# Performance work log

Measured on AMD Instinct MI355X. Metric: run time of the kernel, lower is better.

Reference implementation:

```python
import jax, jax.numpy as jnp
import numpy as np

N = 50000      # atoms
E = 800000     # edges (avg degree 32)
H = 64         # hidden_channels
F = 64         # num_filters
G = 50         # num_gaussians
L = 6          # num_interactions
B = 128        # graphs in batch
MAX_Z = 100
CUTOFF = 10.0


def setup_inputs() -> dict:
    key = jax.random.key(0)
    ks = jax.random.split(key, 20)
    s = 0.05  # weight scale
    return {
        "z": jax.random.randint(ks[0], (N,), 0, MAX_Z, dtype=jnp.int32),
        "pos": jax.random.uniform(ks[1], (N, 3), dtype=jnp.float32) * 5.0,
        "batch": jnp.sort(jax.random.randint(ks[2], (N,), 0, B, dtype=jnp.int32)),
        "edge_index": jax.random.randint(ks[3], (2, E), 0, N, dtype=jnp.int32),
        "embed": jax.random.normal(ks[4], (MAX_Z, H), dtype=jnp.float32) * s,
        "mlp_w1": jax.random.normal(ks[5], (L, G, F), dtype=jnp.float32) * s,
        "mlp_b1": jax.random.normal(ks[6], (L, F), dtype=jnp.float32) * s,
        "mlp_w2": jax.random.normal(ks[7], (L, F, F), dtype=jnp.float32) * s,
        "mlp_b2": jax.random.normal(ks[8], (L, F), dtype=jnp.float32) * s,
        "lin_w": jax.random.normal(ks[9], (L, H, F), dtype=jnp.float32) * s,
        "lin_out_w": jax.random.normal(ks[10], (L, F, H), dtype=jnp.float32) * s,
        "lin_out_b": jax.random.normal(ks[11], (L, H), dtype=jnp.float32) * s,
        "fc1_w": jax.random.normal(ks[12], (H, H // 2), dtype=jnp.float32) * s,
        "fc1_b": jax.random.normal(ks[13], (H // 2,), dtype=jnp.float32) * s,
        "fc2_w": jax.random.normal(ks[14], (H // 2, 1), dtype=jnp.float32) * s,
        "fc2_b": jax.random.normal(ks[15], (1,), dtype=jnp.float32) * s,
    }


def reference(z, pos, batch, edge_index, embed, mlp_w1, mlp_b1, mlp_w2, mlp_b2,
              lin_w, lin_out_w, lin_out_b, fc1_w, fc1_b, fc2_w, fc2_b):
    src, dst = edge_index[0], edge_index[1]
    # edge distances (replaces the python cdist loop; edge list is precomputed)
    d = jnp.sqrt(jnp.sum((pos[src] - pos[dst]) ** 2, axis=-1))  # [E]
    # Gaussian smearing
    offset = jnp.linspace(0.0, CUTOFF, G)
    coeff = -0.5 / (offset[1] - offset[0]) ** 2
    edge_attr = jnp.exp(coeff * (d[:, None] - offset) ** 2)  # [E, G]
    # cosine cutoff
    cut = 0.5 * (jnp.cos(d * np.pi / CUTOFF) + 1.0) * (d < CUTOFF).astype(d.dtype)  # [E]

    h = embed[z]  # [N, H]
    for l in range(L):
        # filter MLP on edge features, modulated by cutoff
        W = jnp.tanh(edge_attr @ mlp_w1[l] + mlp_b1[l]) @ mlp_w2[l] + mlp_b2[l]  # [E, F]
        W = W * cut[:, None]
        h_j = h @ lin_w[l]  # [N, F]
        messages = h_j[src] * W  # gather + modulate  [E, F]
        agg = jax.ops.segment_sum(messages, dst, num_segments=N)  # scatter-add [N, F]
        h = h + (agg @ lin_out_w[l] + lin_out_b[l])  # residual

    # global mean pool over graphs
    sums = jax.ops.segment_sum(h, batch, num_segments=B)  # [B, H]
    cnt = jax.ops.segment_sum(jnp.ones((h.shape[0],), h.dtype), batch, num_segments=B)
    pooled = sums / jnp.maximum(cnt, 1.0)[:, None]

    x = jax.nn.relu(pooled @ fc1_w + fc1_b)  # dropout = identity (eval)
    return x @ fc2_w + fc2_b  # [B, 1]
```

## Files before the change

kernel.cpp:

```cpp
#include <hip/hip_runtime.h>
#include <hip/hip_fp16.h>
#include <math.h>

#define E_EDGES 800000
#define N_ATOMS 50000
#define N_GRAPH 128
#define P_TBL   2048
#define SCAN_NB 49

static constexpr float PI_F   = 3.14159265358979323846f;
static constexpr float GSTEP  = 10.0f / 49.0f;
static constexpr float GCOEFF = -0.5f / (GSTEP * GSTEP);
static constexpr float DMAX   = 8.6603f;
static constexpr float DSCALE = (float)(P_TBL - 1) / DMAX;

__global__ void hist_kernel(const int* __restrict__ dst, int* __restrict__ cnt) {
    int e = blockIdx.x * 256 + threadIdx.x;
    if (e < E_EDGES) atomicAdd(&cnt[dst[e]], 1);
}

__global__ __launch_bounds__(1024)
void scan1_kernel(const int* __restrict__ cnt, int* __restrict__ local_ex,
                  int* __restrict__ bsum) {
    __shared__ int sh[1024];
    const int t = threadIdx.x;
    const int i = blockIdx.x * 1024 + t;
    const int v = (i < N_ATOMS) ? cnt[i] : 0;
    sh[t] = v;
    __syncthreads();
    #pragma unroll
    for (int off = 1; off < 1024; off <<= 1) {
        int u = (t >= off) ? sh[t - off] : 0;
        __syncthreads();
        sh[t] += u;
        __syncthreads();
    }
    if (i < N_ATOMS) local_ex[i] = sh[t] - v;
    if (t == 1023) bsum[blockIdx.x] = sh[t];
}

__global__ __launch_bounds__(1024)
void scan2_kernel(const int* __restrict__ local_ex, const int* __restrict__ bsum,
                  int* __restrict__ starts, int* __restrict__ cursor) {
    __shared__ int off;
    const int b = blockIdx.x;
    if (threadIdx.x < 64) {
        int v = (threadIdx.x < b) ? bsum[threadIdx.x] : 0;
        #pragma unroll
        for (int d = 32; d > 0; d >>= 1) v += __shfl_down(v, d, 64);
        if (threadIdx.x == 0) off = v;
    }
    __syncthreads();
    const int i = b * 1024 + threadIdx.x;
    if (i < N_ATOMS) {
        int v = local_ex[i] + off;
        starts[i] = v;
        cursor[i] = v;
    }
}

__global__ void scatter_kernel(const int* __restrict__ ei, const float* __restrict__ pos,
                               int* __restrict__ cursor, uint2* __restrict__ pk) {
    int e = blockIdx.x * 256 + threadIdx.x;
    if (e >= E_EDGES) return;
    int sidx = ei[e];
    int dd   = ei[E_EDGES + e];
    float dx = pos[3*sidx+0] - pos[3*dd+0];
    float dy = pos[3*sidx+1] - pos[3*dd+1];
    float dz = pos[3*sidx+2] - pos[3*dd+2];
    float dist = sqrtf(dx*dx + dy*dy + dz*dz);
    int p = atomicAdd(&cursor[dd], 1);
    pk[p] = make_uint2((unsigned)sidx, __float_as_uint(dist));
}

__global__ __launch_bounds__(256)
void table_kernel(const float* __restrict__ w1, const float* __restrict__ b1,
                  const float* __restrict__ w2, const float* __restrict__ b2,
                  float* __restrict__ tbl2) {
    __shared__ float sa[4][52];
    __shared__ float st[4][64];
    const int l  = blockIdx.x >> 9;
    const int rb = blockIdx.x & 511;
    const int rr = threadIdx.x >> 6;
    const int f  = threadIdx.x & 63;
    const int r  = rb * 4 + rr;
    const float dp = (float)r * (DMAX / (float)(P_TBL - 1));

    if (f < 50) {
        float t = dp - (float)f * GSTEP;
        sa[rr][f] = expf(GCOEFF * t * t);
    }
    __syncthreads();

    const float* W1 = w1 + (size_t)l * 50 * 64;
    const float* W2 = w2 + (size_t)l * 64 * 64;
    float t = b1[l * 64 + f];
    #pragma unroll 5
    for (int g = 0; g < 50; ++g) t = fmaf(sa[rr][g], W1[g * 64 + f], t);
    st[rr][f] = tanhf(t);
    __syncthreads();

    float w = b2[l * 64 + f];
    #pragma unroll 8
    for (int k = 0; k < 64; ++k) w = fmaf(st[rr][k], W2[k * 64 + f], w);
    float cutv = 0.5f * (cosf(dp * (PI_F / 10.0f)) + 1.0f);
    float val = w * cutv;
    const size_t base = ((size_t)l * P_TBL + r) * 64 + f;
    tbl2[base * 2 + 0] = val;
    if (r > 0) tbl2[(base - 64) * 2 + 1] = val;
}

__device__ __forceinline__ void store_half8(__half* dst, const float* v) {
    union { ushort u[8]; uint4 q; } p;
    #pragma unroll
    for (int j = 0; j < 8; ++j) p.u[j] = __half_as_ushort(__float2half(v[j]));
    *(uint4*)dst = p.q;
}

__global__ __launch_bounds__(256)
void embed_lin0_kernel(const int* __restrict__ z, const float* __restrict__ embed,
                       const float* __restrict__ W,
                       float* __restrict__ h, __half* __restrict__ hj) {
    __shared__ float sA[64 * 65];
    __shared__ float sW[64 * 64];
    const int tid = threadIdx.x;
    const int rbase = blockIdx.x * 64;

    for (int i = tid; i < 64 * 64; i += 256) sW[i] = W[i];
    for (int i = tid; i < 64 * 64; i += 256) {
        int r = i >> 6, k = i & 63;
        int row = rbase + r;
        float v = 0.0f;
        if (row < N_ATOMS) {
            v = embed[(size_t)z[row] * 64 + k];
            h[(size_t)row * 64 + k] = v;
        }
        sA[r * 65 + k] = v;
    }
    __syncthreads();

    const int f0 = (tid & 7) * 8;
    const int r0 = (tid >> 3) * 2;
    float acc[2][8];
    #pragma unroll
    for (int i = 0; i < 2; ++i)
        #pragma unroll
        for (int j = 0; j < 8; ++j) acc[i][j] = 0.0f;

    #pragma unroll 4
    for (int k = 0; k < 64; ++k) {
        float a[2] = { sA[(r0+0)*65 + k], sA[(r0+1)*65 + k] };
        float4 wa = *(const float4*)&sW[k * 64 + f0];
        float4 wb = *(const float4*)&sW[k * 64 + f0 + 4];
        float w[8] = {wa.x, wa.y, wa.z, wa.w, wb.x, wb.y, wb.z, wb.w};
        #pragma unroll
        for (int i = 0; i < 2; ++i)
            #pragma unroll
            for (int j = 0; j < 8; ++j)
                acc[i][j] = fmaf(a[i], w[j], acc[i][j]);
    }

    #pragma unroll
    for (int i = 0; i < 2; ++i) {
        int row = rbase + r0 + i;
        if (row < N_ATOMS)
            store_half8(hj + (size_t)row * 64 + f0, acc[i]);
    }
}

__device__ __forceinline__ float edge_w2(const float2* __restrict__ tbl, float dist, int f) {
    float x = dist * DSCALE;
    int i0 = (int)x; i0 = (i0 > P_TBL - 2) ? (P_TBL - 2) : i0;
    float fr = x - (float)i0;
    float2 t = tbl[i0 * 64 + f];
    return fmaf(fr, t.y - t.x, t.x);
}

__global__ __launch_bounds__(512)
void layer_kernel(const uint2* __restrict__ pk,
                  const int* __restrict__ starts, const int* __restrict__ cnts,
                  const __half* __restrict__ hj_in, const float2* __restrict__ tbl,
                  const float* __restrict__ Wout, const float* __restrict__ bout,
                  float* __restrict__ h,
                  const float* __restrict__ Wlin, __half* __restrict__ hj_out,
                  int doLin) {
    __shared__ float sA[64 * 65];
    __shared__ float sW1[64 * 64];
    __shared__ float sW2[64 * 64];
    __shared__ float sb[64];
    const int tid = threadIdx.x;
    const int rbase = blockIdx.x * 64;
    const int f  = tid & 63;
    const int wv = tid >> 6;
    const int r0 = tid >> 3;
    const int f0 = (tid & 7) * 8;
    const int myrow = rbase + r0;

    float4 hA = make_float4(0.f,0.f,0.f,0.f), hB = hA;
    if (myrow < N_ATOMS) {
        const float* hr = h + (size_t)myrow * 64;
        hA = *(const float4*)&hr[f0];
        hB = *(const float4*)&hr[f0 + 4];
    }

    for (int i = tid; i < 64 * 64; i += 512) sW1[i] = Wout[i];
    if (doLin)
        for (int i = tid; i < 64 * 64; i += 512) sW2[i] = Wlin[i];
    if (tid < 64) sb[tid] = bout[tid];
    __syncthreads();

    for (int i = 0; i < 8; ++i) {
        const int r = wv * 8 + i;
        const int n = rbase + r;
        float res = 0.0f;
        if (n < N_ATOMS) {
            const int s   = starts[n];
            const int end = s + cnts[n];
            float a0 = 0.0f, a1 = 0.0f, a2 = 0.0f, a3 = 0.0f;
            float a4 = 0.0f, a5 = 0.0f, a6 = 0.0f, a7 = 0.0f;
            int e = s;
            for (; e + 8 <= end; e += 8) {
                uint2 p0 = pk[e+0], p1 = pk[e+1], p2 = pk[e+2], p3 = pk[e+3];
                uint2 p4 = pk[e+4], p5 = pk[e+5], p6 = pk[e+6], p7 = pk[e+7];
                float w0 = edge_w2(tbl, __uint_as_float(p0.y), f);
                float w1 = edge_w2(tbl, __uint_as_float(p1.y), f);
                float w2 = edge_w2(tbl, __uint_as_float(p2.y), f);
                float w3 = edge_w2(tbl, __uint_as_float(p3.y), f);
                float w4 = edge_w2(tbl, __uint_as_float(p4.y), f);
                float w5 = edge_w2(tbl, __uint_as_float(p5.y), f);
                float w6 = edge_w2(tbl, __uint_as_float(p6.y), f);
                float w7 = edge_w2(tbl, __uint_as_float(p7.y), f);
                a0 = fmaf(w0, __half2float(hj_in[(size_t)p0.x * 64 + f]), a0);
                a1 = fmaf(w1, __half2float(hj_in[(size_t)p1.x * 64 + f]), a1);
                a2 = fmaf(w2, __half2float(hj_in[(size_t)p2.x * 64 + f]), a2);
                a3 = fmaf(w3, __half2float(hj_in[(size_t)p3.x * 64 + f]), a3);
                a4 = fmaf(w4, __half2float(hj_in[(size_t)p4.x * 64 + f]), a4);
                a5 = fmaf(w5, __half2float(hj_in[(size_t)p5.x * 64 + f]), a5);
                a6 = fmaf(w6, __half2float(hj_in[(size_t)p6.x * 64 + f]), a6);
                a7 = fmaf(w7, __half2float(hj_in[(size_t)p7.x * 64 + f]), a7);
            }
            for (; e + 2 <= end; e += 2) {
                uint2 p0 = pk[e], p1 = pk[e+1];
                float w0 = edge_w2(tbl, __uint_as_float(p0.y), f);
                float w1 = edge_w2(tbl, __uint_as_float(p1.y), f);
                a0 = fmaf(w0, __half2float(hj_in[(size_t)p0.x * 64 + f]), a0);
                a1 = fmaf(w1, __half2float(hj_in[(size_t)p1.x * 64 + f]), a1);
            }
            if (e < end) {
                uint2 p0 = pk[e];
                float w0 = edge_w2(tbl, __uint_as_float(p0.y), f);
                a0 = fmaf(w0, __half2float(hj_in[(size_t)p0.x * 64 + f]), a0);
            }
            res = ((a0 + a1) + (a2 + a3)) + ((a4 + a5) + (a6 + a7));
        }
        sA[r * 65 + f] = res;
    }
    __builtin_amdgcn_wave_barrier();

    float acc[8];
    acc[0] = hA.x + sb[f0+0]; acc[1] = hA.y + sb[f0+1];
    acc[2] = hA.z + sb[f0+2]; acc[3] = hA.w + sb[f0+3];
    acc[4] = hB.x + sb[f0+4]; acc[5] = hB.y + sb[f0+5];
    acc[6] = hB.z + sb[f0+6]; acc[7] = hB.w + sb[f0+7];

    #pragma unroll 4
    for (int k = 0; k < 64; ++k) {
        float a = sA[r0 * 65 + k];
        float4 wa = *(const float4*)&sW1[k * 64 + f0];
        float4 wb = *(const float4*)&sW1[k * 64 + f0 + 4];
        acc[0] = fmaf(a, wa.x, acc[0]); acc[1] = fmaf(a, wa.y, acc[1]);
        acc[2] = fmaf(a, wa.z, acc[2]); acc[3] = fmaf(a, wa.w, acc[3]);
        acc[4] = fmaf(a, wb.x, acc[4]); acc[5] = fmaf(a, wb.y, acc[5]);
        acc[6] = fmaf(a, wb.z, acc[6]); acc[7] = fmaf(a, wb.w, acc[7]);
    }
    __builtin_amdgcn_wave_barrier();

    if (myrow < N_ATOMS) {
        float* o = h + (size_t)myrow * 64;
        *(float4*)&o[f0]     = make_float4(acc[0], acc[1], acc[2], acc[3]);
        *(float4*)&o[f0 + 4] = make_float4(acc[4], acc[5], acc[6], acc[7]);
    }
    #pragma unroll
    for (int j = 0; j < 8; ++j) sA[r0 * 65 + f0 + j] = acc[j];
    if (!doLin) return;
    __builtin_amdgcn_wave_barrier();

    float acc2[8];
    #pragma unroll
    for (int j = 0; j < 8; ++j) acc2[j] = 0.0f;

    #pragma unroll 4
    for (int k = 0; k < 64; ++k) {
        float a = sA[r0 * 65 + k];
        float4 wa = *(const float4*)&sW2[k * 64 + f0];
        float4 wb = *(const float4*)&sW2[k * 64 + f0 + 4];
        acc2[0] = fmaf(a, wa.x, acc2[0]); acc2[1] = fmaf(a, wa.y, acc2[1]);
        acc2[2] = fmaf(a, wa.z, acc2[2]); acc2[3] = fmaf(a, wa.w, acc2[3]);
        acc2[4] = fmaf(a, wb.x, acc2[4]); acc2[5] = fmaf(a, wb.y, acc2[5]);
        acc2[6] = fmaf(a, wb.z, acc2[6]); acc2[7] = fmaf(a, wb.w, acc2[7]);
    }

    if (myrow < N_ATOMS)
        store_half8(hj_out + (size_t)myrow * 64 + f0, acc2);
}

__global__ __launch_bounds__(256)
void pool_head_kernel(const float* __restrict__ h, const int* __restrict__ batch,
                      const float* __restrict__ fc1w, const float* __restrict__ fc1b,
                      const float* __restrict__ fc2w, const float* __restrict__ fc2b,
                      float* __restrict__ out) {
    __shared__ float part[4][64];
    __shared__ float sp[64];
    __shared__ float sx[32];
    __shared__ int bounds[2];
    const int g   = blockIdx.x;
    const int tid = threadIdx.x;

    if (tid < 2) {
        int target = g + tid;
        int lo = 0, hi = N_ATOMS;
        while (lo < hi) {
            int m = (lo + hi) >> 1;
            if (batch[m] < target) lo = m + 1; else hi = m;
        }
        bounds[tid] = lo;
    }
    __syncthreads();
    const int s = bounds[0], epos = bounds[1];

    const int f = tid & 63, wv = tid >> 6;
    float a = 0.0f;
    for (int r = s + wv; r < epos; r += 4) a += h[(size_t)r * 64 + f];
    part[wv][f] = a;
    __syncthreads();

    if (tid < 64) {
        float cnt = (float)(epos - s);
        sp[tid] = (part[0][tid] + part[1][tid] + part[2][tid] + part[3][tid])
                  / fmaxf(cnt, 1.0f);
    }
    __syncthreads();
    if (tid < 32) {
        float a1 = fc1b[tid];
        #pragma unroll 8
        for (int k = 0; k < 64; ++k) a1 = fmaf(sp[k], fc1w[k * 32 + tid], a1);
        sx[tid] = fmaxf(a1, 0.0f);
    }
    __syncthreads();
    if (tid == 0) {
        float a2 = fc2b[0];
        #pragma unroll 8
        for (int j = 0; j < 32; ++j) a2 = fmaf(sx[j], fc2w[j], a2);
        out[g] = a2;
    }
}

extern "C" void kernel_launch(void* const* d_in, const int* in_sizes, int n_in,
                              void* d_out, int out_size, void* d_ws, size_t ws_size,
                              hipStream_t stream) {
    const int*   z         = (const int*)  d_in[0];
    const float* pos       = (const float*)d_in[1];
    const int*   batch     = (const int*)  d_in[2];
    const int*   ei        = (const int*)  d_in[3];
    const float* embed     = (const float*)d_in[4];
    const float* mlp_w1    = (const float*)d_in[5];
    const float* mlp_b1    = (const float*)d_in[6];
    const float* mlp_w2    = (const float*)d_in[7];
    const float* mlp_b2    = (const float*)d_in[8];
    const float* lin_w     = (const float*)d_in[9];
    const float* lin_out_w = (const float*)d_in[10];
    const float* lin_out_b = (const float*)d_in[11];
    const float* fc1w      = (const float*)d_in[12];
    const float* fc1b      = (const float*)d_in[13];
    const float* fc2w      = (const float*)d_in[14];
    const float* fc2b      = (const float*)d_in[15];
    float* out = (float*)d_out;

    char* base = (char*)d_ws;
    const size_t HB = (size_t)N_ATOMS * 64 * sizeof(float);
    const size_t HJ = (size_t)N_ATOMS * 64 * sizeof(__half);
    float*  h     = (float*)base;
    __half* hj0   = (__half*)(base + HB);
    __half* hj1   = (__half*)(base + HB + HJ);
    float2* tbl   = (float2*)(base + HB + 2 * HJ);
    uint2*  pk    = (uint2*)(tbl + (size_t)6 * P_TBL * 64);
    int*    hist  = (int*)(pk + E_EDGES);
    int*    starts= hist  + N_ATOMS;
    int*    cursor= starts+ N_ATOMS;
    int*    lex   = cursor+ N_ATOMS;
    int*    bsum  = lex   + N_ATOMS;

    const int* dst = ei + E_EDGES;

    hipMemsetAsync(hist, 0, N_ATOMS * sizeof(int), stream);
    hist_kernel<<<E_EDGES / 256, 256, 0, stream>>>(dst, hist);
    scan1_kernel<<<SCAN_NB, 1024, 0, stream>>>(hist, lex, bsum);
    scan2_kernel<<<SCAN_NB, 1024, 0, stream>>>(lex, bsum, starts, cursor);
    scatter_kernel<<<E_EDGES / 256, 256, 0, stream>>>(ei, pos, cursor, pk);
    table_kernel<<<6 * (P_TBL / 4), 256, 0, stream>>>(mlp_w1, mlp_b1, mlp_w2, mlp_b2,
                                                      (float*)tbl);

    const int ngemm_grid = (N_ATOMS + 63) / 64;

    embed_lin0_kernel<<<ngemm_grid, 256, 0, stream>>>(z, embed, lin_w, h, hj0);

    __half* hjbuf[2] = { hj0, hj1 };
    for (int l = 0; l < 6; ++l) {
        layer_kernel<<<ngemm_grid, 512, 0, stream>>>(
            pk, starts, hist, hjbuf[l & 1], tbl + (size_t)l * P_TBL * 64,
            lin_out_w + (size_t)l * 64 * 64, lin_out_b + (size_t)l * 64, h,
            (l < 5) ? (lin_w + (size_t)(l + 1) * 64 * 64) : nullptr,
            hjbuf[(l + 1) & 1], (l < 5) ? 1 : 0);
    }

    pool_head_kernel<<<N_GRAPH, 256, 0, stream>>>(h, batch, fc1w, fc1b, fc2w, fc2b, out);
}
```

Measured before the change: 707.7 us.

## Flatten per-wave edge loop across 8 atoms with prefetch; half-precision LDS weights

New measurement: 1.174 ms. 65.9% more time.

```diff
diff --git a/kernel.cpp b/kernel.cpp
--- a/kernel.cpp
+++ b/kernel.cpp
@@ -7,6 +7,7 @@
 #define N_GRAPH 128
 #define P_TBL   2048
 #define SCAN_NB 49
+#define NPB     32
 
 static constexpr float PI_F   = 3.14159265358979323846f;
 static constexpr float GSTEP  = 10.0f / 49.0f;
@@ -51,6 +52,7 @@
         if (threadIdx.x == 0) off = v;
     }
     __syncthreads();
+    if (b == 0 && threadIdx.x == 0) starts[N_ATOMS] = E_EDGES;
     const int i = b * 1024 + threadIdx.x;
     if (i < N_ATOMS) {
         int v = local_ex[i] + off;
@@ -176,20 +178,19 @@
     return fmaf(fr, t.y - t.x, t.x);
 }
 
-__global__ __launch_bounds__(512)
-void layer_kernel(const uint2* __restrict__ pk,
-                  const int* __restrict__ starts, const int* __restrict__ cnts,
+__global__ __launch_bounds__(256)
+void layer_kernel(const uint2* __restrict__ pk, const int* __restrict__ starts,
                   const __half* __restrict__ hj_in, const float2* __restrict__ tbl,
                   const float* __restrict__ Wout, const float* __restrict__ bout,
                   float* __restrict__ h,
                   const float* __restrict__ Wlin, __half* __restrict__ hj_out,
                   int doLin) {
-    __shared__ float sA[64 * 65];
-    __shared__ float sW1[64 * 64];
-    __shared__ float sW2[64 * 64];
-    __shared__ float sb[64];
+    __shared__ float  sA[NPB * 65];
+    __shared__ __half sW1[64 * 64];
+    __shared__ __half sW2[64 * 64];
+    __shared__ float  sb[64];
     const int tid = threadIdx.x;
-    const int rbase = blockIdx.x * 64;
+    const int rbase = blockIdx.x * NPB;
     const int f  = tid & 63;
     const int wv = tid >> 6;
     const int r0 = tid >> 3;
@@ -203,57 +204,59 @@
         hB = *(const float4*)&hr[f0 + 4];
     }
 
-    for (int i = tid; i < 64 * 64; i += 512) sW1[i] = Wout[i];
+    for (int i = tid; i < 64 * 64; i += 256) sW1[i] = __float2half(Wout[i]);
     if (doLin)
-        for (int i = tid; i < 64 * 64; i += 512) sW2[i] = Wlin[i];
+        for (int i = tid; i < 64 * 64; i += 256) sW2[i] = __float2half(Wlin[i]);
     if (tid < 64) sb[tid] = bout[tid];
     __syncthreads();
 
-    for (int i = 0; i < 8; ++i) {
-        const int r = wv * 8 + i;
-        const int n = rbase + r;
+    {
+        const int nbase = rbase + wv * 8;
+        #define BND(i) starts[(nbase + (i) < N_ATOMS) ? (nbase + (i)) : N_ATOMS]
+        const int b0 = BND(0);
+        const int b1 = BND(1), b2 = BND(2), b3 = BND(3), b4 = BND(4);
+        const int b5 = BND(5), b6 = BND(6), b7 = BND(7), b8 = BND(8);
+        #undef BND
+        int e = b0;
+        const int eE = b8;
+        int cur = 0;
         float res = 0.0f;
-        if (n < N_ATOMS) {
-            const int s   = starts[n];
-            const int end = s + cnts[n];
-            float a0 = 0.0f, a1 = 0.0f, a2 = 0.0f, a3 = 0.0f;
-            float a4 = 0.0f, a5 = 0.0f, a6 = 0.0f, a7 = 0.0f;
-            int e = s;
-            for (; e + 8 <= end; e += 8) {
-                uint2 p0 = pk[e+0], p1 = pk[e+1], p2 = pk[e+2], p3 = pk[e+3];
-                uint2 p4 = pk[e+4], p5 = pk[e+5], p6 = pk[e+6], p7 = pk[e+7];
-                float w0 = edge_w2(tbl, __uint_as_float(p0.y), f);
-                float w1 = edge_w2(tbl, __uint_as_float(p1.y), f);
-                float w2 = edge_w2(tbl, __uint_as_float(p2.y), f);
-                float w3 = edge_w2(tbl, __uint_as_float(p3.y), f);
-                float w4 = edge_w2(tbl, __uint_as_float(p4.y), f);
-                float w5 = edge_w2(tbl, __uint_as_float(p5.y), f);
-                float w6 = edge_w2(tbl, __uint_as_float(p6.y), f);
-                float w7 = edge_w2(tbl, __uint_as_float(p7.y), f);
-                a0 = fmaf(w0, __half2float(hj_in[(size_t)p0.x * 64 + f]), a0);
-                a1 = fmaf(w1, __half2float(hj_in[(size_t)p1.x * 64 + f]), a1);
-                a2 = fmaf(w2, __half2float(hj_in[(size_t)p2.x * 64 + f]), a2);
-                a3 = fmaf(w3, __half2float(hj_in[(size_t)p3.x * 64 + f]), a3);
-                a4 = fmaf(w4, __half2float(hj_in[(size_t)p4.x * 64 + f]), a4);
-                a5 = fmaf(w5, __half2float(hj_in[(size_t)p5.x * 64 + f]), a5);
-                a6 = fmaf(w6, __half2float(hj_in[(size_t)p6.x * 64 + f]), a6);
-                a7 = fmaf(w7, __half2float(hj_in[(size_t)p7.x * 64 + f]), a7);
+
+        uint2 p0,p1,p2,p3,p4,p5,p6,p7;
+        int m = eE - e; if (m > 8) m = 8;
+        if (m > 0) p0 = pk[e+0]; if (m > 1) p1 = pk[e+1];
+        if (m > 2) p2 = pk[e+2]; if (m > 3) p3 = pk[e+3];
+        if (m > 4) p4 = pk[e+4]; if (m > 5) p5 = pk[e+5];
+        if (m > 6) p6 = pk[e+6]; if (m > 7) p7 = pk[e+7];
+
+        while (e < eE) {
+            int mn = eE - (e + 8); if (mn > 8) mn = 8;
+            uint2 q0,q1,q2,q3,q4,q5,q6,q7;
+            if (mn > 0) q0 = pk[e+8+0]; if (mn > 1) q1 = pk[e+8+1];
+            if (mn > 2) q2 = pk[e+8+2]; if (mn > 3) q3 = pk[e+8+3];
+            if (mn > 4) q4 = pk[e+8+4]; if (mn > 5) q5 = pk[e+8+5];
+            if (mn > 6) q6 = pk[e+8+6]; if (mn > 7) q7 = pk[e+8+7];
+
+            float v[8];
+            #define GV(j, pj) if (m > j) { \
+                float w = edge_w2(tbl, __uint_as_float(pj.y), f); \
+                v[j] = w * __half2float(hj_in[(size_t)pj.x * 64 + f]); }
+            GV(0,p0) GV(1,p1) GV(2,p2) GV(3,p3) GV(4,p4) GV(5,p5) GV(6,p6) GV(7,p7)
+            #undef GV
+
+            #pragma unroll
+            for (int j = 0; j < 8; ++j) {
+                if (j < m) {
+                    int q = e + j;
+                    int idx = (q>=b1)+(q>=b2)+(q>=b3)+(q>=b4)+(q>=b5)+(q>=b6)+(q>=b7);
+                    while (cur < idx) { sA[(wv*8+cur)*65 + f] = res; res = 0.0f; ++cur; }
+                    res += v[j];
+                }
             }
-            for (; e + 2 <= end; e += 2) {
-                uint2 p0 = pk[e], p1 = pk[e+1];
-                float w0 = edge_w2(tbl, __uint_as_float(p0.y), f);
-                float w1 = edge_w2(tbl, __uint_as_float(p1.y), f);
-                a0 = fmaf(w0, __half2float(hj_in[(size_t)p0.x * 64 + f]), a0);
-                a1 = fmaf(w1, __half2float(hj_in[(size_t)p1.x * 64 + f]), a1);
-            }
-            if (e < end) {
-                uint2 p0 = pk[e];
-                float w0 = edge_w2(tbl, __uint_as_float(p0.y), f);
-                a0 = fmaf(w0, __half2float(hj_in[(size_t)p0.x * 64 + f]), a0);
-            }
-            res = ((a0 + a1) + (a2 + a3)) + ((a4 + a5) + (a6 + a7));
+            e += 8; m = mn;
+            p0=q0; p1=q1; p2=q2; p3=q3; p4=q4; p5=q5; p6=q6; p7=q7;
         }
-        sA[r * 65 + f] = res;
+        while (cur < 8) { sA[(wv*8+cur)*65 + f] = res; res = 0.0f; ++cur; }
     }
     __builtin_amdgcn_wave_barrier();
 
@@ -266,12 +269,16 @@
     #pragma unroll 4
     for (int k = 0; k < 64; ++k) {
         float a = sA[r0 * 65 + k];
-        float4 wa = *(const float4*)&sW1[k * 64 + f0];
-        float4 wb = *(const float4*)&sW1[k * 64 + f0 + 4];
-        acc[0] = fmaf(a, wa.x, acc[0]); acc[1] = fmaf(a, wa.y, acc[1]);
-        acc[2] = fmaf(a, wa.z, acc[2]); acc[3] = fmaf(a, wa.w, acc[3]);
-        acc[4] = fmaf(a, wb.x, acc[4]); acc[5] = fmaf(a, wb.y, acc[5]);
-        acc[6] = fmaf(a, wb.z, acc[6]); acc[7] = fmaf(a, wb.w, acc[7]);
+        union { uint4 q; __half2 h2[4]; } u;
+        u.q = *(const uint4*)&sW1[k * 64 + f0];
+        float2 w0 = __half22float2(u.h2[0]);
+        float2 w1 = __half22float2(u.h2[1]);
+        float2 w2 = __half22float2(u.h2[2]);
+        float2 w3 = __half22float2(u.h2[3]);
+        acc[0] = fmaf(a, w0.x, acc[0]); acc[1] = fmaf(a, w0.y, acc[1]);
+        acc[2] = fmaf(a, w1.x, acc[2]); acc[3] = fmaf(a, w1.y, acc[3]);
+        acc[4] = fmaf(a, w2.x, acc[4]); acc[5] = fmaf(a, w2.y, acc[5]);
+        acc[6] = fmaf(a, w3.x, acc[6]); acc[7] = fmaf(a, w3.y, acc[7]);
     }
     __builtin_amdgcn_wave_barrier();
 
@@ -292,12 +299,16 @@
     #pragma unroll 4
     for (int k = 0; k < 64; ++k) {
         float a = sA[r0 * 65 + k];
-        float4 wa = *(const float4*)&sW2[k * 64 + f0];
-        float4 wb = *(const float4*)&sW2[k * 64 + f0 + 4];
-        acc2[0] = fmaf(a, wa.x, acc2[0]); acc2[1] = fmaf(a, wa.y, acc2[1]);
-        acc2[2] = fmaf(a, wa.z, acc2[2]); acc2[3] = fmaf(a, wa.w, acc2[3]);
-        acc2[4] = fmaf(a, wb.x, acc2[4]); acc2[5] = fmaf(a, wb.y, acc2[5]);
-        acc2[6] = fmaf(a, wb.z, acc2[6]); acc2[7] = fmaf(a, wb.w, acc2[7]);
+        union { uint4 q; __half2 h2[4]; } u;
+        u.q = *(const uint4*)&sW2[k * 64 + f0];
+        float2 w0 = __half22float2(u.h2[0]);
+        float2 w1 = __half22float2(u.h2[1]);
+        float2 w2 = __half22float2(u.h2[2]);
+        float2 w3 = __half22float2(u.h2[3]);
+        acc2[0] = fmaf(a, w0.x, acc2[0]); acc2[1] = fmaf(a, w0.y, acc2[1]);
+        acc2[2] = fmaf(a, w1.x, acc2[2]); acc2[3] = fmaf(a, w1.y, acc2[3]);
+        acc2[4] = fmaf(a, w2.x, acc2[4]); acc2[5] = fmaf(a, w2.y, acc2[5]);
+        acc2[6] = fmaf(a, w3.x, acc2[6]); acc2[7] = fmaf(a, w3.y, acc2[7]);
     }
 
     if (myrow < N_ATOMS)
@@ -386,7 +397,7 @@
     uint2*  pk    = (uint2*)(tbl + (size_t)6 * P_TBL * 64);
     int*    hist  = (int*)(pk + E_EDGES);
     int*    starts= hist  + N_ATOMS;
-    int*    cursor= starts+ N_ATOMS;
+    int*    cursor= starts+ N_ATOMS + 1;
     int*    lex   = cursor+ N_ATOMS;
     int*    bsum  = lex   + N_ATOMS;
 
@@ -400,14 +411,13 @@
     table_kernel<<<6 * (P_TBL / 4), 256, 0, stream>>>(mlp_w1, mlp_b1, mlp_w2, mlp_b2,
                                                       (float*)tbl);
 
-    const int ngemm_grid = (N_ATOMS + 63) / 64;
-
-    embed_lin0_kernel<<<ngemm_grid, 256, 0, stream>>>(z, embed, lin_w, h, hj0);
-
+    embed_lin0_kernel<<<(N_ATOMS + 63) / 64, 256, 0, stream>>>(z, embed, lin_w, h, hj0);
+
+    const int layer_grid = (N_ATOMS + NPB - 1) / NPB;
     __half* hjbuf[2] = { hj0, hj1 };
     for (int l = 0; l < 6; ++l) {
-        layer_kernel<<<ngemm_grid, 512, 0, stream>>>(
-            pk, starts, hist, hjbuf[l & 1], tbl + (size_t)l * P_TBL * 64,
+        layer_kernel<<<layer_grid, 256, 0, stream>>>(
+            pk, starts, hjbuf[l & 1], tbl + (size_t)l * P_TBL * 64,
             lin_out_w + (size_t)l * 64 * 64, lin_out_b + (size_t)l * 64, h,
             (l < 5) ? (lin_w + (size_t)(l + 1) * 64 * 64) : nullptr,
             hjbuf[(l + 1) & 1], (l < 5) ? 1 : 0);
```
